# Performance work log

Measured on AMD Instinct MI355X. Metric: run time of the kernel, lower is better.

## Reference

```python
import jax, jax.numpy as jnp
import numpy as np

B, S, D, H = 2, 2048, 2048, 16
DH = D // H  # 128
ROPE_BASE = 10000.0


def setup_inputs() -> dict:
    key = jax.random.key(0)
    ks = jax.random.split(key, 5)
    scale = 0.02
    return {
        "x": jax.random.normal(ks[0], (B, S, D), dtype=jnp.float32),
        "wq": jax.random.normal(ks[1], (D, D), dtype=jnp.float32) * scale,
        "wk": jax.random.normal(ks[2], (D, D), dtype=jnp.float32) * scale,
        "wv": jax.random.normal(ks[3], (D, D), dtype=jnp.float32) * scale,
        "wo": jax.random.normal(ks[4], (D, D), dtype=jnp.float32) * scale,
    }


def _rope_cache(seq_len, dhead):
    # flash-attn RotaryEmbedding: inv_freq over even dims, full rotary_dim = dhead
    inv_freq = 1.0 / (ROPE_BASE ** (jnp.arange(0, dhead, 2, dtype=jnp.float32) / dhead))
    t = jnp.arange(seq_len, dtype=jnp.float32)
    freqs = jnp.einsum("s,d->sd", t, inv_freq)  # [S, DH/2]
    return jnp.cos(freqs), jnp.sin(freqs)


def _apply_rope_interleaved(t, cos, sin):
    # t: [B, S, H, DH]; interleaved pairs (t[...,0::2], t[...,1::2])
    te, to = t[..., 0::2], t[..., 1::2]
    c = cos[None, :, None, :]
    s = sin[None, :, None, :]
    re = te * c - to * s
    ro = te * s + to * c
    return jnp.stack([re, ro], axis=-1).reshape(t.shape)


def reference(x, wq, wk, wv, wo):
    b, s, d = x.shape
    q = (x @ wq).reshape(b, s, H, DH)
    k = (x @ wk).reshape(b, s, H, DH)
    v = (x @ wv).reshape(b, s, H, DH)

    cos, sin = _rope_cache(s, DH)
    q = _apply_rope_interleaved(q.astype(jnp.float32), cos, sin)
    k = _apply_rope_interleaved(k.astype(jnp.float32), cos, sin)

    # flash_attn_func(causal=True) semantics: bf16 inputs, fp32 softmax, scale 1/sqrt(dhead)
    qb = q.astype(jnp.bfloat16)
    kb = k.astype(jnp.bfloat16)
    vb = v.astype(jnp.bfloat16)
    scale = 1.0 / np.sqrt(DH)
    scores = jnp.einsum("bqhd,bkhd->bhqk", qb, kb,
                        preferred_element_type=jnp.float32) * scale
    causal = jnp.tril(jnp.ones((s, s), dtype=bool))
    scores = jnp.where(causal[None, None], scores, -jnp.inf)
    p = jax.nn.softmax(scores, axis=-1)  # fp32
    attn = jnp.einsum("bhqk,bkhd->bqhd", p.astype(jnp.bfloat16), vb,
                      preferred_element_type=jnp.float32)
    attn = attn.astype(jnp.bfloat16).astype(x.dtype)  # flash returns bf16, then .to(x)
    out = attn.reshape(b, s, d) @ wo
    return out
```

## Files before the change

### kernel.cpp

```cpp
#include <hip/hip_runtime.h>
#include <hip/hip_bf16.h>
#include <stdint.h>

#define B_SZ   2
#define S_LEN  2048
#define DMODEL 2048
#define NH     16
#define DHD    128

typedef __attribute__((ext_vector_type(8))) __bf16 bf16x8;
typedef __attribute__((ext_vector_type(4))) float  f32x4;
typedef __attribute__((ext_vector_type(4))) float  float4v;
typedef __attribute__((ext_vector_type(8))) unsigned short ushort8;
typedef __attribute__((ext_vector_type(4))) unsigned short ushort4v;

__device__ __forceinline__ unsigned short f2bf(float f) {
  unsigned int u = __float_as_uint(f);
  unsigned int r = (u + 0x7fffu + ((u >> 16) & 1u)) >> 16;
  return (unsigned short)r;
}

__device__ __forceinline__ unsigned int cvt_pk_bf16(float lo, float hi) {
  unsigned int r;
  asm("v_cvt_pk_bf16_f32 %0, %1, %2" : "=v"(r) : "v"(lo), "v"(hi));
  return r;
}

__device__ __forceinline__ void async_cp16(void* lds, const void* g) {
  __builtin_amdgcn_global_load_lds(
      (const __attribute__((address_space(1))) void*)g,
      (__attribute__((address_space(3))) void*)lds, 16, 0, 0);
}

__global__ __launch_bounds__(256) void k_cast_bf16(const float* __restrict__ in,
                                                   unsigned short* __restrict__ out,
                                                   int n4) {
  int i = blockIdx.x * 256 + threadIdx.x;
  if (i >= n4) return;
  float4v v = ((const float4v*)in)[i];
  ushort4v o;
  o[0] = f2bf(v[0]); o[1] = f2bf(v[1]); o[2] = f2bf(v[2]); o[3] = f2bf(v[3]);
  ((ushort4v*)out)[i] = o;
}

__global__ __launch_bounds__(256) void k_transpose_cast(const float* __restrict__ W,
                                                        unsigned short* __restrict__ WT) {
  __shared__ unsigned short tile[64 * 72];
  const int n0 = blockIdx.x * 64;
  const int k0 = blockIdx.y * 64;
  const int t = threadIdx.x;
#pragma unroll
  for (int i = 0; i < 4; ++i) {
    int c = t + 256 * i;
    int r = c >> 4, c4 = c & 15;
    float4v v = *(const float4v*)(W + (size_t)(k0 + r) * DMODEL + n0 + c4 * 4);
    ushort4v o;
    o[0] = f2bf(v[0]); o[1] = f2bf(v[1]); o[2] = f2bf(v[2]); o[3] = f2bf(v[3]);
    *(ushort4v*)(&tile[r * 72 + c4 * 4]) = o;
  }
  __syncthreads();
#pragma unroll
  for (int i = 0; i < 2; ++i) {
    int c = t + 256 * i;
    int n = c >> 3, k8 = c & 7;
    ushort8 o;
#pragma unroll
    for (int j = 0; j < 8; ++j) o[j] = tile[(k8 * 8 + j) * 72 + n];
    *(ushort8*)(WT + (size_t)(n0 + n) * DMODEL + k0 + k8 * 8) = o;
  }
}

__global__ __launch_bounds__(256) void k_rope_table(float* __restrict__ cosT,
                                                    float* __restrict__ sinT) {
  int i = blockIdx.x * 256 + threadIdx.x;
  int s = i >> 6, dj = i & 63;
  float e = __expf(-9.210340371976184f * (float)dj * (1.0f / 64.0f));
  float f = (float)s * e;
  cosT[i] = cosf(f);
  sinT[i] = sinf(f);
}

#define GNT 32

template <int EPI>
__global__ __launch_bounds__(512, 2) void k_gemm256(
    const unsigned short* __restrict__ A,
    const unsigned short* __restrict__ BT,
    float* __restrict__ C0,
    unsigned short* __restrict__ Cq,
    unsigned short* __restrict__ Ck,
    unsigned short* __restrict__ Cv,
    const float* __restrict__ cosT,
    const float* __restrict__ sinT,
    int NBN) {
  __shared__ char smem[131072];
  const int tid = threadIdx.x;

  const int nwg = gridDim.x;
  const int wg = blockIdx.x;
  const int swz = (wg & 7) * (nwg >> 3) + (wg >> 3);
  const int bn = swz % NBN, bm = swz / NBN;

  const int s8 = tid & 7;
  const int r5 = (tid >> 3) & 31;
  const int hf = tid >> 8;
  const int r7 = tid >> 3;
  const int gs = s8 ^ (r7 & 7);
  const unsigned short* Abase = A + (size_t)(bm * 256 + hf * 128 + r5) * 2048 + gs * 8;
  const unsigned short* Bbase = BT + (size_t)(bn * 256 + r7) * 2048 + gs * 8;
  const int dstA = tid * 16;
  const int dstB = 32768 + tid * 16;

  const int lane = tid & 63, wid = tid >> 6;
  const int wr = wid >> 2, wc = wid & 3;
  const int lr = lane & 15, hi = lane >> 4;
  const int cx = (lr & 7) << 4;
  const int ck0 = (hi * 16) ^ cx;
  const int ck1 = (64 + hi * 16) ^ cx;
  const int aRB = wr * 4096 + lr * 128;
  const int bRB = 32768 + (wc >> 1) * 16384 + ((wc & 1) * 64 + lr) * 128;

  f32x4 acc[8][4];
#pragma unroll
  for (int m = 0; m < 8; ++m)
#pragma unroll
    for (int n = 0; n < 4; ++n) {
      f32x4 z = {0.f, 0.f, 0.f, 0.f};
      acc[m][n] = z;
    }

#define STAGE_A(c, G, t_) do {                                              \
    const unsigned short* _src = Abase + (size_t)(G) * 64 * 2048 + (t_) * 64; \
    async_cp16(smem + (c) * 65536 + (G) * 16384 + dstA, _src);              \
    async_cp16(smem + (c) * 65536 + (G) * 16384 + dstA + 8192, _src + 32 * 2048); \
  } while (0)
#define STAGE_B(c, u, t_) do {                                              \
    const unsigned short* _src = Bbase + (size_t)(u) * 128 * 2048 + (t_) * 64; \
    async_cp16(smem + (c) * 65536 + (u) * 16384 + dstB, _src);              \
    async_cp16(smem + (c) * 65536 + (u) * 16384 + dstB + 8192, _src + 64 * 2048); \
  } while (0)

#define TILEBODY(CC) do {                                                   \
    bf16x8 bfr[4][2];                                                       \
    _Pragma("unroll")                                                       \
    for (int p = 0; p < 4; ++p) {                                           \
      bf16x8 a00 = *(const bf16x8*)(smem + (CC) * 65536 + aRB + p * 8192 + ck0); \
      bf16x8 a01 = *(const bf16x8*)(smem + (CC) * 65536 + aRB + p * 8192 + ck1); \
      bf16x8 a10 = *(const bf16x8*)(smem + (CC) * 65536 + aRB + p * 8192 + 2048 + ck0); \
      bf16x8 a11 = *(const bf16x8*)(smem + (CC) * 65536 + aRB + p * 8192 + 2048 + ck1); \
      if (p == 0) {                                                         \
        _Pragma("unroll")                                                   \
        for (int n = 0; n < 4; ++n) {                                       \
          bfr[n][0] = *(const bf16x8*)(smem + (CC) * 65536 + bRB + n * 2048 + ck0); \
          bfr[n][1] = *(const bf16x8*)(smem + (CC) * 65536 + bRB + n * 2048 + ck1); \
        }                                                                   \
      }                                                                     \
      if (p == 0 && t + 1 < GNT) STAGE_A((CC) ^ 1, 1, t + 1);               \
      if (p == 1 && t + 2 < GNT) STAGE_B(CC, 0, t + 2);                     \
      if (p == 2 && t + 2 < GNT) STAGE_B(CC, 1, t + 2);                     \
      if (p == 3 && t + 2 < GNT) STAGE_A(CC, 0, t + 2);                     \
      __builtin_amdgcn_s_barrier();                                         \
      asm volatile("s_waitcnt lgkmcnt(0)" ::: "memory");                    \
      __builtin_amdgcn_sched_barrier(0);                                    \
      __builtin_amdgcn_s_setprio(1);                                        \
      _Pragma("unroll")                                                     \
      for (int n = 0; n < 4; ++n) {                                         \
        acc[2 * p][n]     = __builtin_amdgcn_mfma_f32_16x16x32_bf16(a00, bfr[n][0], acc[2 * p][n], 0, 0, 0); \
        acc[2 * p][n]     = __builtin_amdgcn_mfma_f32_16x16x32_bf16(a01, bfr[n][1], acc[2 * p][n], 0, 0, 0); \
        acc[2 * p + 1][n] = __builtin_amdgcn_mfma_f32_16x16x32_bf16(a10, bfr[n][0], acc[2 * p + 1][n], 0, 0, 0); \
        acc[2 * p + 1][n] = __builtin_amdgcn_mfma_f32_16x16x32_bf16(a11, bfr[n][1], acc[2 * p + 1][n], 0, 0, 0); \
      }                                                                     \
      __builtin_amdgcn_s_setprio(0);                                        \
      if (p == 3) {                                                         \
        if (t + 2 < GNT) { asm volatile("s_waitcnt vmcnt(6)" ::: "memory"); } \
        else             { asm volatile("s_waitcnt vmcnt(0)" ::: "memory"); } \
      }                                                                     \
      __builtin_amdgcn_s_barrier();                                         \
      __builtin_amdgcn_sched_barrier(0);                                    \
    }                                                                       \
  } while (0)

  STAGE_A(0, 0, 0); STAGE_A(0, 1, 0); STAGE_B(0, 0, 0); STAGE_B(0, 1, 0);
  STAGE_B(1, 0, 1); STAGE_B(1, 1, 1); STAGE_A(1, 0, 1);
  asm volatile("s_waitcnt vmcnt(6)" ::: "memory");
  __builtin_amdgcn_s_barrier();
  __builtin_amdgcn_sched_barrier(0);

  int t;
  for (int it = 0; it < GNT / 2; ++it) {
    t = 2 * it;     TILEBODY(0);
    t = 2 * it + 1; TILEBODY(1);
  }

  const int row_b = bm * 256 + wr * 128 + hi * 4;
  const int col_b = bn * 256 + wc * 64 + lr;
  if (EPI == 0) {
#pragma unroll
    for (int m = 0; m < 8; ++m)
#pragma unroll
      for (int n = 0; n < 4; ++n) {
        int col = col_b + n * 16;
#pragma unroll
        for (int j = 0; j < 4; ++j) {
          int row = row_b + m * 16 + j;
          C0[(size_t)row * 2048 + col] = acc[m][n][j];
        }
      }
  } else {
    const int sel = bn >> 3;
#pragma unroll
    for (int m = 0; m < 8; ++m) {
#pragma unroll
      for (int n = 0; n < 4; ++n) {
        int col = col_b + n * 16;
        int hh = (col >> 7) & 15, d = col & 127;
        if (sel == 2) {
#pragma unroll
          for (int j = 0; j < 4; ++j) {
            int row = row_b + m * 16 + j;
            int b = row >> 11, s = row & 2047;
            Cv[((size_t)(b * NH + hh) * S_LEN + s) * DHD + d] = f2bf(acc[m][n][j]);
          }
        } else {
          unsigned short* dst = sel ? Ck : Cq;
          int dj = d >> 1;
          float sgn = (d & 1) ? 1.f : -1.f;
#pragma unroll
          for (int j = 0; j < 4; ++j) {
            int row = row_b + m * 16 + j;
            int b = row >> 11, s = row & 2047;
            float v = acc[m][n][j];
            float pp = __shfl_xor(v, 1);
            float cc = cosT[(s << 6) + dj];
            float sn = sinT[(s << 6) + dj];
            dst[((size_t)(b * NH + hh) * S_LEN + s) * DHD + d] = f2bf(v * cc + sgn * pp * sn);
          }
        }
      }
    }
  }
#undef TILEBODY
#undef STAGE_A
#undef STAGE_B
}

__global__ __launch_bounds__(256) void k_flash_attn(const unsigned short* __restrict__ Qg,
                                                    const unsigned short* __restrict__ Kg,
                                                    const unsigned short* __restrict__ Vg,
                                                    unsigned short* __restrict__ Og) {
  __shared__ unsigned short K_lds[2][64 * 128];
  __shared__ unsigned short VT_lds[2][128 * 64];

  const int pq = blockIdx.x, h = blockIdx.y, b = blockIdx.z;
  const int t = threadIdx.x;
  const int lane = t & 63, wave = t >> 6;
  const int hi = lane >> 4, lr = lane & 15;

  const size_t head = (size_t)(b * NH + h) * (size_t)(S_LEN * DHD);
  const unsigned short* Q = Qg + head;
  const unsigned short* Kp = Kg + head;
  const unsigned short* Vp = Vg + head;

  const int kr0 = t >> 4;
  const int kgc = (t & 15) ^ (kr0 & 7);
  const unsigned short* Kbase = Kp + (size_t)kr0 * DHD + kgc * 8;
  const int kdst = t * 16;

  const int vdc = t & 15, vsp0 = t >> 4;
  const unsigned short* Vbase = Vp + (size_t)(2 * vsp0) * DHD + vdc * 8;
  const int bo0 = 16 * ((vsp0 >> 1) & 3) + 8 * ((vsp0 >> 3) & 1) + 4 * (vsp0 & 1);

  const float sc = 0.08838834764831845f;

  for (int pass = 0; pass < 2; ++pass) {
    const int qt = (pass == 0) ? pq : (31 - pq);
    const int nt = qt + 1;
    const int qbase = qt * 64 + wave * 16;
    const int qrow = qbase + lr;

    bf16x8 qf[4];
    {
      const unsigned short* qr_ = Q + (size_t)(qbase + lr) * DHD;
#pragma unroll
      for (int kc = 0; kc < 4; ++kc) qf[kc] = *(const bf16x8*)(qr_ + kc * 32 + hi * 8);
    }

    f32x4 of[8];
#pragma unroll
    for (int i = 0; i < 8; ++i) {
      f32x4 z = {0.f, 0.f, 0.f, 0.f};
      of[i] = z;
    }
    float mS = -INFINITY;
    float lsum = 0.f;

    {
#pragma unroll
      for (int i = 0; i < 4; ++i)
        async_cp16((char*)K_lds[0] + kdst + i * 4096, Kbase + (size_t)(16 * i) * DHD);
      ushort8 va0 = *(const ushort8*)(Vbase);
      ushort8 vb0 = *(const ushort8*)(Vbase + DHD);
      ushort8 va1 = *(const ushort8*)(Vbase + (size_t)32 * DHD);
      ushort8 vb1 = *(const ushort8*)(Vbase + (size_t)33 * DHD);
#pragma unroll
      for (int j = 0; j < 8; ++j) {
        int row = vdc * 8 + j;
        int swz = ((j ^ vdc) & 7) << 4;
        *(unsigned int*)((char*)VT_lds[0] + row * 128 + (bo0 ^ swz)) =
            (unsigned int)va0[j] | ((unsigned int)vb0[j] << 16);
        *(unsigned int*)((char*)VT_lds[0] + row * 128 + ((bo0 | 64) ^ swz)) =
            (unsigned int)va1[j] | ((unsigned int)vb1[j] << 16);
      }
    }
    __syncthreads();

    for (int tt = 0; tt < nt; ++tt) {
      const int cur = tt & 1;
      const int kv0 = tt * 64;
      const bool more = (tt + 1 < nt);
      const bool diag = (tt == qt);

      ushort8 va0, vb0, va1, vb1;
      if (more) {
        const unsigned short* ks = Kbase + (size_t)(kv0 + 64) * DHD;
#pragma unroll
        for (int i = 0; i < 4; ++i)
          async_cp16((char*)K_lds[cur ^ 1] + kdst + i * 4096, ks + (size_t)(16 * i) * DHD);
        const unsigned short* vs = Vbase + (size_t)(kv0 + 64) * DHD;
        va0 = *(const ushort8*)(vs);
        vb0 = *(const ushort8*)(vs + DHD);
        va1 = *(const ushort8*)(vs + (size_t)32 * DHD);
        vb1 = *(const ushort8*)(vs + (size_t)33 * DHD);
      }

      const char* Kb = (const char*)K_lds[cur];
      f32x4 sf[4];
#pragma unroll
      for (int n = 0; n < 4; ++n) {
        f32x4 z = {0.f, 0.f, 0.f, 0.f};
        sf[n] = z;
      }
      __builtin_amdgcn_s_setprio(1);
#pragma unroll
      for (int n = 0; n < 4; ++n) {
        const int kr = n * 16 + lr;
        const int kswz = (kr & 7) << 4;
#pragma unroll
        for (int kc = 0; kc < 4; ++kc) {
          bf16x8 kf = *(const bf16x8*)(Kb + kr * 256 + ((kc * 64 + hi * 16) ^ kswz));
          sf[n] = __builtin_amdgcn_mfma_f32_16x16x32_bf16(kf, qf[kc], sf[n], 0, 0, 0);
        }
      }
      __builtin_amdgcn_s_setprio(0);

      float p[4][4];
      float mx = -INFINITY;
      if (diag) {
#pragma unroll
        for (int n = 0; n < 4; ++n)
#pragma unroll
          for (int j = 0; j < 4; ++j) {
            int kvcol = kv0 + n * 16 + hi * 4 + j;
            float v = (kvcol > qrow) ? -INFINITY : sf[n][j];
            p[n][j] = v;
            mx = fmaxf(mx, v);
          }
      } else {
#pragma unroll
        for (int n = 0; n < 4; ++n)
#pragma unroll
          for (int j = 0; j < 4; ++j) {
            float v = sf[n][j];
            p[n][j] = v;
            mx = fmaxf(mx, v);
          }
      }
      mx = fmaxf(mx, __shfl_xor(mx, 16));
      mx = fmaxf(mx, __shfl_xor(mx, 32));
      float mn = fmaxf(mS, mx);
      float corr = __expf((mS - mn) * sc);
      mS = mn;
      float mns = mn * sc;
      float rs = 0.f;
#pragma unroll
      for (int n = 0; n < 4; ++n)
#pragma unroll
        for (int j = 0; j < 4; ++j) {
          float e = __expf(__builtin_fmaf(p[n][j], sc, -mns));
          p[n][j] = e;
          rs += e;
        }
      rs += __shfl_xor(rs, 16);
      rs += __shfl_xor(rs, 32);
      lsum = lsum * corr + rs;

      unsigned int pk[4][2];
#pragma unroll
      for (int n = 0; n < 4; ++n) {
        pk[n][0] = cvt_pk_bf16(p[n][0], p[n][1]);
        pk[n][1] = cvt_pk_bf16(p[n][2], p[n][3]);
      }

      float corrb[4];
#pragma unroll
      for (int j = 0; j < 4; ++j) corrb[j] = __shfl(corr, hi * 4 + j);
#pragma unroll
      for (int nd = 0; nd < 8; ++nd)
#pragma unroll
        for (int j = 0; j < 4; ++j) of[nd][j] *= corrb[j];

      const char* Vb = (const char*)VT_lds[cur];
      __builtin_amdgcn_s_setprio(1);
#pragma unroll
      for (int kc = 0; kc < 2; ++kc) {
        union { unsigned int u[4]; bf16x8 v; } pa;
        pa.u[0] = pk[2 * kc][0];
        pa.u[1] = pk[2 * kc][1];
        pa.u[2] = pk[2 * kc + 1][0];
        pa.u[3] = pk[2 * kc + 1][1];
#pragma unroll
        for (int nd = 0; nd < 8; ++nd) {
          const int vr = nd * 16 + lr;
          const int vswz = ((vr & 7) ^ ((vr >> 3) & 7)) << 4;
          bf16x8 vf = *(const bf16x8*)(Vb + vr * 128 + ((kc * 64 + hi * 16) ^ vswz));
          of[nd] = __builtin_amdgcn_mfma_f32_16x16x32_bf16(pa.v, vf, of[nd], 0, 0, 0);
        }
      }
      __builtin_amdgcn_s_setprio(0);

      if (more) {
        char* Vw = (char*)VT_lds[cur ^ 1];
#pragma unroll
        for (int j = 0; j < 8; ++j) {
          int row = vdc * 8 + j;
          int swz = ((j ^ vdc) & 7) << 4;
          *(unsigned int*)(Vw + row * 128 + (bo0 ^ swz)) =
              (unsigned int)va0[j] | ((unsigned int)vb0[j] << 16);
          *(unsigned int*)(Vw + row * 128 + ((bo0 | 64) ^ swz)) =
              (unsigned int)va1[j] | ((unsigned int)vb1[j] << 16);
        }
      }
      __syncthreads();
    }

    float inv[4];
#pragma unroll
    for (int j = 0; j < 4; ++j) {
      float ls = __shfl(lsum, hi * 4 + j);
      inv[j] = 1.0f / ls;
    }
#pragma unroll
    for (int nd = 0; nd < 8; ++nd)
#pragma unroll
      for (int j = 0; j < 4; ++j) {
        int qr = qbase + hi * 4 + j;
        Og[((size_t)(b * S_LEN + qr) * NH + h) * DHD + nd * 16 + lr] = f2bf(of[nd][j] * inv[j]);
      }
  }
}

extern "C" void kernel_launch(void* const* d_in, const int* in_sizes, int n_in,
                              void* d_out, int out_size, void* d_ws, size_t ws_size,
                              hipStream_t stream) {
  const float* x  = (const float*)d_in[0];
  const float* wq = (const float*)d_in[1];
  const float* wk = (const float*)d_in[2];
  const float* wv = (const float*)d_in[3];
  const float* wo = (const float*)d_in[4];
  float* out = (float*)d_out;

  char* ws = (char*)d_ws;
  unsigned short* xb    = (unsigned short*)(ws);
  unsigned short* wqT   = (unsigned short*)(ws + 16777216);
  unsigned short* wkT   = (unsigned short*)(ws + 25165824);
  unsigned short* wvT   = (unsigned short*)(ws + 33554432);
  unsigned short* woT   = (unsigned short*)(ws + 41943040);
  unsigned short* qb    = (unsigned short*)(ws + 50331648);
  unsigned short* kb    = (unsigned short*)(ws + 67108864);
  unsigned short* vb    = (unsigned short*)(ws + 83886080);
  float*          cosT  = (float*)(ws + 100663296);
  float*          sinT  = (float*)(ws + 101187584);
  unsigned short* attnb = xb;

  k_cast_bf16<<<8192, 256, 0, stream>>>(x, xb, 2097152);
  dim3 tg(32, 32);
  k_transpose_cast<<<tg, 256, 0, stream>>>(wq, wqT);
  k_transpose_cast<<<tg, 256, 0, stream>>>(wk, wkT);
  k_transpose_cast<<<tg, 256, 0, stream>>>(wv, wvT);
  k_transpose_cast<<<tg, 256, 0, stream>>>(wo, woT);
  k_rope_table<<<512, 256, 0, stream>>>(cosT, sinT);

  k_gemm256<1><<<384, 512, 0, stream>>>(xb, wqT, nullptr, qb, kb, vb, cosT, sinT, 24);

  dim3 ga(16, 16, 2);
  k_flash_attn<<<ga, 256, 0, stream>>>(qb, kb, vb, attnb);

  k_gemm256<0><<<128, 512, 0, stream>>>(attnb, woT, out, nullptr, nullptr, nullptr,
                                        nullptr, nullptr, 8);
}
```

Measured before the change: 277.9 us.

## Shrink GEMM tiles to 128x256, restructure pipeline, batch weight transposes

Replaces the 256x256-tile GEMM with a 128x256-tile variant that uses a two-phase k-split MFMA schedule, precomputed swizzled LDS offsets, and an XCD-aware block mapping. The grid doubles (768 and 256 workgroups), which should fill the 256 CUs better, especially for the output projection that previously launched only 128 blocks. The four weight transpose-cast launches are merged into one launch using blockIdx.z, cutting launch overhead. Smaller tiles lower per-block data reuse and raise global/L2 traffic, and the new waitcnt/barrier schedule could expose latency.

```diff
diff --git a/kernel.cpp b/kernel.cpp
--- a/kernel.cpp
+++ b/kernel.cpp
@@ -43,9 +43,15 @@
   ((ushort4v*)out)[i] = o;
 }
 
-__global__ __launch_bounds__(256) void k_transpose_cast(const float* __restrict__ W,
-                                                        unsigned short* __restrict__ WT) {
+__global__ __launch_bounds__(256) void k_transpose_all(const float* __restrict__ w0,
+                                                       const float* __restrict__ w1,
+                                                       const float* __restrict__ w2,
+                                                       const float* __restrict__ w3,
+                                                       unsigned short* __restrict__ WTbase) {
   __shared__ unsigned short tile[64 * 72];
+  const int z = blockIdx.z;
+  const float* W = (z == 0) ? w0 : (z == 1) ? w1 : (z == 2) ? w2 : w3;
+  unsigned short* WT = WTbase + (size_t)z * 4194304;
   const int n0 = blockIdx.x * 64;
   const int k0 = blockIdx.y * 64;
   const int t = threadIdx.x;
@@ -80,10 +86,8 @@
   sinT[i] = sinf(f);
 }
 
-#define GNT 32
-
 template <int EPI>
-__global__ __launch_bounds__(512, 2) void k_gemm256(
+__global__ __launch_bounds__(512, 2) void k_gemm128(
     const unsigned short* __restrict__ A,
     const unsigned short* __restrict__ BT,
     float* __restrict__ C0,
@@ -92,111 +96,123 @@
     unsigned short* __restrict__ Cv,
     const float* __restrict__ cosT,
     const float* __restrict__ sinT,
-    int NBN) {
-  __shared__ char smem[131072];
+    int chn) {
+  __shared__ char smem[98304];
   const int tid = threadIdx.x;
 
-  const int nwg = gridDim.x;
-  const int wg = blockIdx.x;
-  const int swz = (wg & 7) * (nwg >> 3) + (wg >> 3);
-  const int bn = swz % NBN, bm = swz / NBN;
-
-  const int s8 = tid & 7;
-  const int r5 = (tid >> 3) & 31;
-  const int hf = tid >> 8;
-  const int r7 = tid >> 3;
-  const int gs = s8 ^ (r7 & 7);
-  const unsigned short* Abase = A + (size_t)(bm * 256 + hf * 128 + r5) * 2048 + gs * 8;
-  const unsigned short* Bbase = BT + (size_t)(bn * 256 + r7) * 2048 + gs * 8;
+  const int xcd = blockIdx.x & 7;
+  const int idx = blockIdx.x >> 3;
+  const int bm = (xcd >> 2) * 16 + (idx & 15);
+  const int bn = (xcd & 3) * chn + (idx >> 4);
+
+  const int gs = (tid & 7) ^ ((tid >> 3) & 7);
+  const unsigned short* Abase = A + (size_t)(bm * 128 + (tid >> 3)) * 2048 + gs * 8;
+  const unsigned short* Bbase = BT + (size_t)(bn * 256 + (tid >> 3)) * 2048 + gs * 8;
   const int dstA = tid * 16;
-  const int dstB = 32768 + tid * 16;
+  const int dstB = 16384 + tid * 16;
 
   const int lane = tid & 63, wid = tid >> 6;
-  const int wr = wid >> 2, wc = wid & 3;
+  const int wr = wid >> 2, wcn = wid & 3;
   const int lr = lane & 15, hi = lane >> 4;
-  const int cx = (lr & 7) << 4;
-  const int ck0 = (hi * 16) ^ cx;
-  const int ck1 = (64 + hi * 16) ^ cx;
-  const int aRB = wr * 4096 + lr * 128;
-  const int bRB = 32768 + (wc >> 1) * 16384 + ((wc & 1) * 64 + lr) * 128;
-
-  f32x4 acc[8][4];
-#pragma unroll
-  for (int m = 0; m < 8; ++m)
+  int aoff[4][2], boff[4][2];
+#pragma unroll
+  for (int m = 0; m < 4; ++m) {
+    int row = wr * 64 + m * 16 + lr;
+#pragma unroll
+    for (int k = 0; k < 2; ++k)
+      aoff[m][k] = row * 128 + ((((k * 4 + hi)) ^ (row & 7)) << 4);
+  }
+#pragma unroll
+  for (int n = 0; n < 4; ++n) {
+    int row = wcn * 64 + n * 16 + lr;
+#pragma unroll
+    for (int k = 0; k < 2; ++k)
+      boff[n][k] = 16384 + row * 128 + ((((k * 4 + hi)) ^ (row & 7)) << 4);
+  }
+
+  f32x4 acc[4][4];
+#pragma unroll
+  for (int m = 0; m < 4; ++m)
 #pragma unroll
     for (int n = 0; n < 4; ++n) {
       f32x4 z = {0.f, 0.f, 0.f, 0.f};
       acc[m][n] = z;
     }
 
-#define STAGE_A(c, G, t_) do {                                              \
-    const unsigned short* _src = Abase + (size_t)(G) * 64 * 2048 + (t_) * 64; \
-    async_cp16(smem + (c) * 65536 + (G) * 16384 + dstA, _src);              \
-    async_cp16(smem + (c) * 65536 + (G) * 16384 + dstA + 8192, _src + 32 * 2048); \
+#define STG_A(c, t_) do {                                                   \
+    const unsigned short* _s = Abase + (t_) * 64;                           \
+    async_cp16(smem + (c) * 49152 + dstA, _s);                              \
+    async_cp16(smem + (c) * 49152 + dstA + 8192, _s + 64 * 2048);           \
   } while (0)
-#define STAGE_B(c, u, t_) do {                                              \
-    const unsigned short* _src = Bbase + (size_t)(u) * 128 * 2048 + (t_) * 64; \
-    async_cp16(smem + (c) * 65536 + (u) * 16384 + dstB, _src);              \
-    async_cp16(smem + (c) * 65536 + (u) * 16384 + dstB + 8192, _src + 64 * 2048); \
+#define STG_B(c, t_) do {                                                   \
+    const unsigned short* _s = Bbase + (t_) * 64;                           \
+    async_cp16(smem + (c) * 49152 + dstB, _s);                              \
+    async_cp16(smem + (c) * 49152 + dstB + 8192, _s + 64 * 2048);           \
+    async_cp16(smem + (c) * 49152 + dstB + 16384, _s + 128 * 2048);         \
+    async_cp16(smem + (c) * 49152 + dstB + 24576, _s + 192 * 2048);         \
   } while (0)
 
-#define TILEBODY(CC) do {                                                   \
-    bf16x8 bfr[4][2];                                                       \
-    _Pragma("unroll")                                                       \
-    for (int p = 0; p < 4; ++p) {                                           \
-      bf16x8 a00 = *(const bf16x8*)(smem + (CC) * 65536 + aRB + p * 8192 + ck0); \
-      bf16x8 a01 = *(const bf16x8*)(smem + (CC) * 65536 + aRB + p * 8192 + ck1); \
-      bf16x8 a10 = *(const bf16x8*)(smem + (CC) * 65536 + aRB + p * 8192 + 2048 + ck0); \
-      bf16x8 a11 = *(const bf16x8*)(smem + (CC) * 65536 + aRB + p * 8192 + 2048 + ck1); \
-      if (p == 0) {                                                         \
-        _Pragma("unroll")                                                   \
-        for (int n = 0; n < 4; ++n) {                                       \
-          bfr[n][0] = *(const bf16x8*)(smem + (CC) * 65536 + bRB + n * 2048 + ck0); \
-          bfr[n][1] = *(const bf16x8*)(smem + (CC) * 65536 + bRB + n * 2048 + ck1); \
-        }                                                                   \
-      }                                                                     \
-      if (p == 0 && t + 1 < GNT) STAGE_A((CC) ^ 1, 1, t + 1);               \
-      if (p == 1 && t + 2 < GNT) STAGE_B(CC, 0, t + 2);                     \
-      if (p == 2 && t + 2 < GNT) STAGE_B(CC, 1, t + 2);                     \
-      if (p == 3 && t + 2 < GNT) STAGE_A(CC, 0, t + 2);                     \
-      __builtin_amdgcn_s_barrier();                                         \
-      asm volatile("s_waitcnt lgkmcnt(0)" ::: "memory");                    \
-      __builtin_amdgcn_sched_barrier(0);                                    \
-      __builtin_amdgcn_s_setprio(1);                                        \
-      _Pragma("unroll")                                                     \
-      for (int n = 0; n < 4; ++n) {                                         \
-        acc[2 * p][n]     = __builtin_amdgcn_mfma_f32_16x16x32_bf16(a00, bfr[n][0], acc[2 * p][n], 0, 0, 0); \
-        acc[2 * p][n]     = __builtin_amdgcn_mfma_f32_16x16x32_bf16(a01, bfr[n][1], acc[2 * p][n], 0, 0, 0); \
-        acc[2 * p + 1][n] = __builtin_amdgcn_mfma_f32_16x16x32_bf16(a10, bfr[n][0], acc[2 * p + 1][n], 0, 0, 0); \
-        acc[2 * p + 1][n] = __builtin_amdgcn_mfma_f32_16x16x32_bf16(a11, bfr[n][1], acc[2 * p + 1][n], 0, 0, 0); \
-      }                                                                     \
-      __builtin_amdgcn_s_setprio(0);                                        \
-      if (p == 3) {                                                         \
-        if (t + 2 < GNT) { asm volatile("s_waitcnt vmcnt(6)" ::: "memory"); } \
-        else             { asm volatile("s_waitcnt vmcnt(0)" ::: "memory"); } \
-      }                                                                     \
-      __builtin_amdgcn_s_barrier();                                         \
-      __builtin_amdgcn_sched_barrier(0);                                    \
-    }                                                                       \
-  } while (0)
-
-  STAGE_A(0, 0, 0); STAGE_A(0, 1, 0); STAGE_B(0, 0, 0); STAGE_B(0, 1, 0);
-  STAGE_B(1, 0, 1); STAGE_B(1, 1, 1); STAGE_A(1, 0, 1);
-  asm volatile("s_waitcnt vmcnt(6)" ::: "memory");
+  auto tile = [&](int T, int CC, bool DO_A, bool DO_B, int VM) __attribute__((always_inline)) {
+    const char* Sb = smem + CC * 49152;
+    bf16x8 a0[4], b0[4], a1[4], b1[4];
+#pragma unroll
+    for (int m = 0; m < 4; ++m) a0[m] = *(const bf16x8*)(Sb + aoff[m][0]);
+#pragma unroll
+    for (int n = 0; n < 4; ++n) b0[n] = *(const bf16x8*)(Sb + boff[n][0]);
+    __builtin_amdgcn_sched_barrier(0);
+#pragma unroll
+    for (int m = 0; m < 4; ++m) a1[m] = *(const bf16x8*)(Sb + aoff[m][1]);
+#pragma unroll
+    for (int n = 0; n < 4; ++n) b1[n] = *(const bf16x8*)(Sb + boff[n][1]);
+    if (DO_A) STG_A(CC ^ 1, T + 1);
+    asm volatile("s_waitcnt lgkmcnt(8)" ::: "memory");
+    __builtin_amdgcn_sched_barrier(0);
+    __builtin_amdgcn_s_setprio(1);
+#pragma unroll
+    for (int m = 0; m < 4; ++m)
+#pragma unroll
+      for (int n = 0; n < 4; ++n)
+        acc[m][n] = __builtin_amdgcn_mfma_f32_16x16x32_bf16(a0[m], b0[n], acc[m][n], 0, 0, 0);
+    __builtin_amdgcn_s_setprio(0);
+    __builtin_amdgcn_s_barrier();
+    __builtin_amdgcn_sched_barrier(0);
+    asm volatile("s_waitcnt lgkmcnt(0)" ::: "memory");
+    __builtin_amdgcn_sched_barrier(0);
+    if (DO_B) STG_B(CC, T + 2);
+    __builtin_amdgcn_s_setprio(1);
+#pragma unroll
+    for (int m = 0; m < 4; ++m)
+#pragma unroll
+      for (int n = 0; n < 4; ++n)
+        acc[m][n] = __builtin_amdgcn_mfma_f32_16x16x32_bf16(a1[m], b1[n], acc[m][n], 0, 0, 0);
+    __builtin_amdgcn_s_setprio(0);
+    if (VM == 0) asm volatile("s_waitcnt vmcnt(4)" ::: "memory");
+    else if (VM == 1) asm volatile("s_waitcnt vmcnt(0)" ::: "memory");
+    if (VM != 2) {
+      __builtin_amdgcn_s_barrier();
+      __builtin_amdgcn_sched_barrier(0);
+    }
+  };
+
+  STG_B(0, 0);
+  STG_A(0, 0);
+  STG_B(1, 1);
+  asm volatile("s_waitcnt vmcnt(4)" ::: "memory");
   __builtin_amdgcn_s_barrier();
   __builtin_amdgcn_sched_barrier(0);
 
-  int t;
-  for (int it = 0; it < GNT / 2; ++it) {
-    t = 2 * it;     TILEBODY(0);
-    t = 2 * it + 1; TILEBODY(1);
-  }
-
-  const int row_b = bm * 256 + wr * 128 + hi * 4;
-  const int col_b = bn * 256 + wc * 64 + lr;
+  for (int it = 0; it < 15; ++it) {
+    tile(2 * it, 0, true, true, 0);
+    tile(2 * it + 1, 1, true, true, 0);
+  }
+  tile(30, 0, true, false, 1);
+  tile(31, 1, false, false, 2);
+
+  const int row_b = bm * 128 + wr * 64 + hi * 4;
+  const int col_b = bn * 256 + wcn * 64 + lr;
   if (EPI == 0) {
 #pragma unroll
-    for (int m = 0; m < 8; ++m)
+    for (int m = 0; m < 4; ++m)
 #pragma unroll
       for (int n = 0; n < 4; ++n) {
         int col = col_b + n * 16;
@@ -209,7 +225,7 @@
   } else {
     const int sel = bn >> 3;
 #pragma unroll
-    for (int m = 0; m < 8; ++m) {
+    for (int m = 0; m < 4; ++m) {
 #pragma unroll
       for (int n = 0; n < 4; ++n) {
         int col = col_b + n * 16;
@@ -239,9 +255,8 @@
       }
     }
   }
-#undef TILEBODY
-#undef STAGE_A
-#undef STAGE_B
+#undef STG_A
+#undef STG_B
 }
 
 __global__ __launch_bounds__(256) void k_flash_attn(const unsigned short* __restrict__ Qg,
@@ -472,8 +487,6 @@
   char* ws = (char*)d_ws;
   unsigned short* xb    = (unsigned short*)(ws);
   unsigned short* wqT   = (unsigned short*)(ws + 16777216);
-  unsigned short* wkT   = (unsigned short*)(ws + 25165824);
-  unsigned short* wvT   = (unsigned short*)(ws + 33554432);
   unsigned short* woT   = (unsigned short*)(ws + 41943040);
   unsigned short* qb    = (unsigned short*)(ws + 50331648);
   unsigned short* kb    = (unsigned short*)(ws + 67108864);
@@ -483,18 +496,15 @@
   unsigned short* attnb = xb;
 
   k_cast_bf16<<<8192, 256, 0, stream>>>(x, xb, 2097152);
-  dim3 tg(32, 32);
-  k_transpose_cast<<<tg, 256, 0, stream>>>(wq, wqT);
-  k_transpose_cast<<<tg, 256, 0, stream>>>(wk, wkT);
-  k_transpose_cast<<<tg, 256, 0, stream>>>(wv, wvT);
-  k_transpose_cast<<<tg, 256, 0, stream>>>(wo, woT);
+  dim3 tg(32, 32, 4);
+  k_transpose_all<<<tg, 256, 0, stream>>>(wq, wk, wv, wo, wqT);
   k_rope_table<<<512, 256, 0, stream>>>(cosT, sinT);
 
-  k_gemm256<1><<<384, 512, 0, stream>>>(xb, wqT, nullptr, qb, kb, vb, cosT, sinT, 24);
+  k_gemm128<1><<<768, 512, 0, stream>>>(xb, wqT, nullptr, qb, kb, vb, cosT, sinT, 6);
 
   dim3 ga(16, 16, 2);
   k_flash_attn<<<ga, 256, 0, stream>>>(qb, kb, vb, attnb);
 
-  k_gemm256<0><<<128, 512, 0, stream>>>(attnb, woT, out, nullptr, nullptr, nullptr,
-                                        nullptr, nullptr, 8);
-}
+  k_gemm128<0><<<256, 512, 0, stream>>>(attnb, woT, out, nullptr, nullptr, nullptr,
+                                        nullptr, nullptr, 2);
+}
```

Result: faster. 240.5 us (-13.5%).
